# Kernel tuning notes

Measured on AMD Instinct MI355X. Metric: run time of the kernel, lower is better.

The kernel has to match this reference:

```python
import jax, jax.numpy as jnp
import numpy as np
import math

STRIDES = {"p3": 8, "p4": 16, "p5": 32}
STRIDE_SCALE = 4
ASPECT_RATIOS = (0.5, 1.0, 2.0)
SCALE_CLAMP = math.log(224.0 / 8.0)
IOU_LOW, IOU_HIGH = 0.3, 0.6
IMG = 784.0


def _make_locations(hw, stride):
    # centers of feature cells projected to image coords
    xs = (jnp.arange(hw, dtype=jnp.float32) + 0.5) * stride
    gy, gx = jnp.meshgrid(xs, xs, indexing="ij")
    return jnp.stack([gx.ravel(), gy.ravel()], axis=1)  # (H*W, 2)


def setup_inputs() -> dict:
    key = jax.random.key(0)
    k1, k2 = jax.random.split(key)
    locations_p3 = _make_locations(98, 8)
    locations_p4 = _make_locations(49, 16)
    locations_p5 = _make_locations(25, 32)
    n_anchors = (9604 + 2401 + 625) * 3  # 37890
    deltas = jax.random.normal(k1, (n_anchors, 4), dtype=jnp.float32) * 0.2
    # GT boxes (M,5): x1,y1,x2,y2,class ; make valid boxes
    km1, km2, km3 = jax.random.split(k2, 3)
    xy1 = jax.random.uniform(km1, (64, 2), minval=0.0, maxval=IMG * 0.7)
    wh = jax.random.uniform(km2, (64, 2), minval=16.0, maxval=IMG * 0.3)
    cls = jax.random.randint(km3, (64, 1), 0, 20).astype(jnp.float32)
    gt_boxes = jnp.concatenate([xy1, xy1 + wh, cls], axis=1)
    return {
        "locations_p3": locations_p3,
        "locations_p4": locations_p4,
        "locations_p5": locations_p5,
        "deltas": deltas,
        "gt_boxes": gt_boxes,
    }


def _anchors_for_level(locations, stride):
    # locations: (L, 2)
    area = (STRIDE_SCALE * stride) ** 2
    boxes = []
    for ar in ASPECT_RATIOS:
        w = math.sqrt(area / ar)
        h = area / w
        xc, yc = locations[:, 0], locations[:, 1]
        boxes.append(jnp.stack([xc - w / 2.0, yc - h / 2.0,
                                xc + w / 2.0, yc + h / 2.0], axis=1))
    # (A, L, 4) -> (L, A, 4) -> (L*A, 4)
    return jnp.stack(boxes).transpose(1, 0, 2).reshape(-1, 4)


def _apply_deltas(deltas, anchors):
    dx, dy = deltas[:, 0], deltas[:, 1]
    dw = jnp.minimum(deltas[:, 2], SCALE_CLAMP)
    dh = jnp.minimum(deltas[:, 3], SCALE_CLAMP)
    wa = anchors[:, 2] - anchors[:, 0]
    ha = anchors[:, 3] - anchors[:, 1]
    xa = anchors[:, 0] + wa / 2.0
    ya = anchors[:, 1] + ha / 2.0
    xp = dx * wa + xa
    yp = dy * ha + ya
    wp = jnp.exp(dw) * wa
    hp = jnp.exp(dh) * ha
    return jnp.stack([xp - wp / 2.0, yp - hp / 2.0,
                      xp + wp / 2.0, yp + hp / 2.0], axis=1)


def _iou(b1, b2):
    a1 = (b1[:, 2] - b1[:, 0]) * (b1[:, 3] - b1[:, 1])
    a2 = (b2[:, 2] - b2[:, 0]) * (b2[:, 3] - b2[:, 1])
    lt = jnp.maximum(b1[:, None, :2], b2[None, :, :2])
    rb = jnp.minimum(b1[:, None, 2:], b2[None, :, 2:])
    wh = jnp.clip(rb - lt, 0.0)
    inter = wh[:, :, 0] * wh[:, :, 1]
    union = a1[:, None] + a2[None, :] - inter
    return inter / union


def _get_deltas(anchors, gt_boxes4):
    invalid = gt_boxes4[:, 0] < 0
    wa = anchors[:, 2] - anchors[:, 0]
    ha = anchors[:, 3] - anchors[:, 1]
    xa = anchors[:, 0] + wa / 2.0
    ya = anchors[:, 1] + ha / 2.0
    wg = jnp.clip(gt_boxes4[:, 2] - gt_boxes4[:, 0], 1.0)
    hg = jnp.clip(gt_boxes4[:, 3] - gt_boxes4[:, 1], 1.0)
    xg = gt_boxes4[:, 0] + wg / 2.0
    yg = gt_boxes4[:, 1] + hg / 2.0
    d = jnp.stack([(xg - xa) / wa, (yg - ya) / ha,
                   jnp.log(wg / wa), jnp.log(hg / ha)], axis=1)
    return jnp.where(invalid[:, None], -1e8, d)


def _match(anchors, gt_boxes):
    # gt_boxes: (M,5). Assume all valid (class != -1) per setup.
    m = _iou(anchors, gt_boxes[:, :4])  # (N, M)
    idx = jnp.argmax(m, axis=1)
    quality = jnp.max(m, axis=1)
    matched = gt_boxes[idx]  # (N, 5)
    matched = jnp.where((quality <= IOU_LOW)[:, None], -1.0, matched)
    neutral = (quality > IOU_LOW) & (quality < IOU_HIGH)
    matched = jnp.where(neutral[:, None], -1e8, matched)
    return matched


def reference(locations_p3, locations_p4, locations_p5, deltas, gt_boxes):
    a3 = _anchors_for_level(locations_p3, STRIDES["p3"])
    a4 = _anchors_for_level(locations_p4, STRIDES["p4"])
    a5 = _anchors_for_level(locations_p5, STRIDES["p5"])
    anchors = jnp.concatenate([a3, a4, a5], axis=0)  # (N, 4)
    proposals = _apply_deltas(deltas, anchors)       # (N, 4)
    matched_gt = _match(anchors, gt_boxes)           # (N, 5)
    gt_deltas = _get_deltas(anchors, matched_gt[:, :4])  # (N, 4)
    return proposals, matched_gt, gt_deltas
```

## Files before the change

kernel.cpp:

```cpp
#include <hip/hip_runtime.h>
#include <math.h>

#define N_LOC3 9604
#define N_LOC4 2401
#define N_LOC5 625
#define N_A3   28812
#define N_A4   36015
#define N_TOTAL 37890
#define N_GT   64

#define SCALE_CLAMP_F 3.3322045101752038f
#define SENTINEL (-100000000.0f)

__global__ __launch_bounds__(256) void rpn_fused_kernel(
    const float* __restrict__ loc3,
    const float* __restrict__ loc4,
    const float* __restrict__ loc5,
    const float* __restrict__ deltas,
    const float* __restrict__ gt,
    float* __restrict__ out)
{
    __shared__ float sgt[N_GT * 5];
    __shared__ float sarea[N_GT];

    const int tid = threadIdx.x;
    for (int i = tid; i < N_GT * 5; i += blockDim.x) sgt[i] = gt[i];
    __syncthreads();
    if (tid < N_GT) {
        sarea[tid] = (sgt[tid*5 + 2] - sgt[tid*5 + 0]) * (sgt[tid*5 + 3] - sgt[tid*5 + 1]);
    }
    __syncthreads();

    const int a = blockIdx.x * blockDim.x + tid;
    if (a >= N_TOTAL) return;

    int stride_i, rel;
    const float* loc;
    if (a < N_A3)      { stride_i = 8;  loc = loc3; rel = a; }
    else if (a < N_A4) { stride_i = 16; loc = loc4; rel = a - N_A3; }
    else               { stride_i = 32; loc = loc5; rel = a - N_A4; }
    const int li = rel / 3;
    const int ar = rel - li * 3;

    const float2 xy = ((const float2*)loc)[li];
    const float xc = xy.x, yc = xy.y;

    const double s4   = 4.0 * (double)stride_i;
    const double area = s4 * s4;
    const double ard  = (ar == 0) ? 0.5 : (ar == 1 ? 1.0 : 2.0);
    const double wd   = sqrt(area / ard);
    const double hd   = area / wd;
    const float hw = (float)(wd * 0.5);
    const float hh = (float)(hd * 0.5);

    const float x1 = xc - hw, y1 = yc - hh;
    const float x2 = xc + hw, y2 = yc + hh;

    const float wa = x2 - x1;
    const float ha = y2 - y1;
    const float xa = x1 + wa * 0.5f;
    const float ya = y1 + ha * 0.5f;

    const float4 d = ((const float4*)deltas)[a];
    const float dw = fminf(d.z, SCALE_CLAMP_F);
    const float dh = fminf(d.w, SCALE_CLAMP_F);
    const float xp = d.x * wa + xa;
    const float yp = d.y * ha + ya;
    const float wp = expf(dw) * wa;
    const float hp = expf(dh) * ha;
    float4 prop;
    prop.x = xp - wp * 0.5f;
    prop.y = yp - hp * 0.5f;
    prop.z = xp + wp * 0.5f;
    prop.w = yp + hp * 0.5f;
    ((float4*)out)[a] = prop;

    const float a1 = wa * ha;
    float best = -1.0f;
    int bidx = 0;
    #pragma unroll 8
    for (int j = 0; j < N_GT; ++j) {
        const float gx1 = sgt[j*5 + 0];
        const float gy1 = sgt[j*5 + 1];
        const float gx2 = sgt[j*5 + 2];
        const float gy2 = sgt[j*5 + 3];
        const float ltx = fmaxf(x1, gx1);
        const float lty = fmaxf(y1, gy1);
        const float rbx = fminf(x2, gx2);
        const float rby = fminf(y2, gy2);
        const float iw = fmaxf(rbx - ltx, 0.0f);
        const float ih = fmaxf(rby - lty, 0.0f);
        const float inter = iw * ih;
        const float uni = a1 + sarea[j] - inter;
        const float iou = inter / uni;
        if (iou > best) { best = iou; bidx = j; }
    }

    float m0, m1, m2, m3, m4;
    if (best <= 0.3f) {
        m0 = m1 = m2 = m3 = m4 = -1.0f;
    } else if (best < 0.6f) {
        m0 = m1 = m2 = m3 = m4 = SENTINEL;
    } else {
        m0 = sgt[bidx*5 + 0];
        m1 = sgt[bidx*5 + 1];
        m2 = sgt[bidx*5 + 2];
        m3 = sgt[bidx*5 + 3];
        m4 = sgt[bidx*5 + 4];
    }
    float* mout = out + N_TOTAL * 4 + a * 5;
    mout[0] = m0; mout[1] = m1; mout[2] = m2; mout[3] = m3; mout[4] = m4;

    float o0, o1, o2, o3;
    if (m0 < 0.0f) {
        o0 = o1 = o2 = o3 = SENTINEL;
    } else {
        const float wg = fmaxf(m2 - m0, 1.0f);
        const float hg = fmaxf(m3 - m1, 1.0f);
        const float xg = m0 + wg * 0.5f;
        const float yg = m1 + hg * 0.5f;
        o0 = (xg - xa) / wa;
        o1 = (yg - ya) / ha;
        o2 = logf(wg / wa);
        o3 = logf(hg / ha);
    }
    float* gout = out + N_TOTAL * 9 + a * 4;
    gout[0] = o0; gout[1] = o1; gout[2] = o2; gout[3] = o3;
}

extern "C" void kernel_launch(void* const* d_in, const int* in_sizes, int n_in,
                              void* d_out, int out_size, void* d_ws, size_t ws_size,
                              hipStream_t stream) {
    const float* loc3   = (const float*)d_in[0];
    const float* loc4   = (const float*)d_in[1];
    const float* loc5   = (const float*)d_in[2];
    const float* deltas = (const float*)d_in[3];
    const float* gt     = (const float*)d_in[4];
    float* out = (float*)d_out;

    const int block = 256;
    const int grid = (N_TOTAL + block - 1) / block;
    rpn_fused_kernel<<<grid, block, 0, stream>>>(loc3, loc4, loc5, deltas, gt, out);
}
```

Baseline: 72.70 us.

## Split GT matching across four lanes per anchor with shuffle reduction

Each anchor is now handled by four threads. Each thread scans 16 of the 64 GT boxes, and the four partial results are combined with xor shuffles. The IoU comparison uses cross-multiplication in place of a division per box, and anchor half-sizes are computed on the host instead of with per-thread double-precision sqrt. Output writes are split across the sub-lanes, which quadruples the thread count and makes the proposal and delta math redundant across the four lanes. The cross-multiplied comparison may break ties differently from the per-box division.

New measurement: 68.08 us. -6.4%, faster.

```diff
diff --git a/kernel.cpp b/kernel.cpp
--- a/kernel.cpp
+++ b/kernel.cpp
@@ -1,65 +1,114 @@
 #include <hip/hip_runtime.h>
 #include <math.h>
 
-#define N_LOC3 9604
-#define N_LOC4 2401
-#define N_LOC5 625
-#define N_A3   28812
-#define N_A4   36015
+#define N_A3    28812
+#define N_A4    36015
 #define N_TOTAL 37890
-#define N_GT   64
+#define N_GT    64
 
 #define SCALE_CLAMP_F 3.3322045101752038f
 #define SENTINEL (-100000000.0f)
 
-__global__ __launch_bounds__(256) void rpn_fused_kernel(
+__global__ __launch_bounds__(256) void rpn_fused_v2(
     const float* __restrict__ loc3,
     const float* __restrict__ loc4,
     const float* __restrict__ loc5,
     const float* __restrict__ deltas,
     const float* __restrict__ gt,
-    float* __restrict__ out)
+    float* __restrict__ out,
+    float hw_a, float hh_a,
+    float hw_c, float hh_c)
 {
     __shared__ float sgt[N_GT * 5];
     __shared__ float sarea[N_GT];
 
     const int tid = threadIdx.x;
-    for (int i = tid; i < N_GT * 5; i += blockDim.x) sgt[i] = gt[i];
-    __syncthreads();
     if (tid < N_GT) {
-        sarea[tid] = (sgt[tid*5 + 2] - sgt[tid*5 + 0]) * (sgt[tid*5 + 3] - sgt[tid*5 + 1]);
+        const float g0 = gt[tid * 5 + 0];
+        const float g1 = gt[tid * 5 + 1];
+        const float g2 = gt[tid * 5 + 2];
+        const float g3 = gt[tid * 5 + 3];
+        const float g4 = gt[tid * 5 + 4];
+        sgt[tid * 5 + 0] = g0; sgt[tid * 5 + 1] = g1; sgt[tid * 5 + 2] = g2;
+        sgt[tid * 5 + 3] = g3; sgt[tid * 5 + 4] = g4;
+        sarea[tid] = (g2 - g0) * (g3 - g1);
     }
     __syncthreads();
 
-    const int a = blockIdx.x * blockDim.x + tid;
+    const int gidx = blockIdx.x * 256 + tid;
+    const int a    = gidx >> 2;
+    const int sub  = tid & 3;
     if (a >= N_TOTAL) return;
 
-    int stride_i, rel;
+    int rel, lvl;
     const float* loc;
-    if (a < N_A3)      { stride_i = 8;  loc = loc3; rel = a; }
-    else if (a < N_A4) { stride_i = 16; loc = loc4; rel = a - N_A3; }
-    else               { stride_i = 32; loc = loc5; rel = a - N_A4; }
+    if (a < N_A3)      { lvl = 0; loc = loc3; rel = a; }
+    else if (a < N_A4) { lvl = 1; loc = loc4; rel = a - N_A3; }
+    else               { lvl = 2; loc = loc5; rel = a - N_A4; }
     const int li = rel / 3;
     const int ar = rel - li * 3;
 
     const float2 xy = ((const float2*)loc)[li];
-    const float xc = xy.x, yc = xy.y;
+    const float scale = (float)(1 << lvl);
+    const float hw = (ar == 0 ? hw_a : (ar == 1 ? 16.0f : hw_c)) * scale;
+    const float hh = (ar == 0 ? hh_a : (ar == 1 ? 16.0f : hh_c)) * scale;
 
-    const double s4   = 4.0 * (double)stride_i;
-    const double area = s4 * s4;
-    const double ard  = (ar == 0) ? 0.5 : (ar == 1 ? 1.0 : 2.0);
-    const double wd   = sqrt(area / ard);
-    const double hd   = area / wd;
-    const float hw = (float)(wd * 0.5);
-    const float hh = (float)(hd * 0.5);
+    const float x1 = xy.x - hw, y1 = xy.y - hh;
+    const float x2 = xy.x + hw, y2 = xy.y + hh;
+    const float wa = x2 - x1, ha = y2 - y1;
+    const float xa = x1 + wa * 0.5f, ya = y1 + ha * 0.5f;
+    const float a1 = wa * ha;
 
-    const float x1 = xc - hw, y1 = yc - hh;
-    const float x2 = xc + hw, y2 = yc + hh;
+    int   bj;
+    float bi, bu;
+    {
+        const int j0 = sub * 16;
+        {
+            const float ltx = fmaxf(x1, sgt[j0 * 5 + 0]);
+            const float lty = fmaxf(y1, sgt[j0 * 5 + 1]);
+            const float rbx = fminf(x2, sgt[j0 * 5 + 2]);
+            const float rby = fminf(y2, sgt[j0 * 5 + 3]);
+            const float iw = fmaxf(rbx - ltx, 0.0f);
+            const float ih = fmaxf(rby - lty, 0.0f);
+            bi = iw * ih;
+            bu = a1 + sarea[j0] - bi;
+            bj = j0;
+        }
+        #pragma unroll
+        for (int k = 1; k < 16; ++k) {
+            const int j = j0 + k;
+            const float ltx = fmaxf(x1, sgt[j * 5 + 0]);
+            const float lty = fmaxf(y1, sgt[j * 5 + 1]);
+            const float rbx = fminf(x2, sgt[j * 5 + 2]);
+            const float rby = fminf(y2, sgt[j * 5 + 3]);
+            const float iw = fmaxf(rbx - ltx, 0.0f);
+            const float ih = fmaxf(rby - lty, 0.0f);
+            const float inter = iw * ih;
+            const float uni = a1 + sarea[j] - inter;
+            if (inter * bu > bi * uni) { bi = inter; bu = uni; bj = j; }
+        }
+    }
+    #pragma unroll
+    for (int s = 1; s < 4; s <<= 1) {
+        const float oi = __shfl_xor(bi, s, 64);
+        const float ou = __shfl_xor(bu, s, 64);
+        const int   oj = __shfl_xor(bj, s, 64);
+        const float p_o = oi * bu, p_b = bi * ou;
+        if (p_o > p_b || (p_o == p_b && oj < bj)) { bi = oi; bu = ou; bj = oj; }
+    }
 
-    const float wa = x2 - x1;
-    const float ha = y2 - y1;
-    const float xa = x1 + wa * 0.5f;
-    const float ya = y1 + ha * 0.5f;
+    const float q = bi / bu;
+
+    float m0, m1, m2, m3, m4;
+    if (q <= 0.3f) {
+        m0 = m1 = m2 = m3 = m4 = -1.0f;
+    } else if (q < 0.6f) {
+        m0 = m1 = m2 = m3 = m4 = SENTINEL;
+    } else {
+        const int off = bj * 5;
+        m0 = sgt[off + 0]; m1 = sgt[off + 1]; m2 = sgt[off + 2];
+        m3 = sgt[off + 3]; m4 = sgt[off + 4];
+    }
 
     const float4 d = ((const float4*)deltas)[a];
     const float dw = fminf(d.z, SCALE_CLAMP_F);
@@ -73,43 +122,6 @@
     prop.y = yp - hp * 0.5f;
     prop.z = xp + wp * 0.5f;
     prop.w = yp + hp * 0.5f;
-    ((float4*)out)[a] = prop;
-
-    const float a1 = wa * ha;
-    float best = -1.0f;
-    int bidx = 0;
-    #pragma unroll 8
-    for (int j = 0; j < N_GT; ++j) {
-        const float gx1 = sgt[j*5 + 0];
-        const float gy1 = sgt[j*5 + 1];
-        const float gx2 = sgt[j*5 + 2];
-        const float gy2 = sgt[j*5 + 3];
-        const float ltx = fmaxf(x1, gx1);
-        const float lty = fmaxf(y1, gy1);
-        const float rbx = fminf(x2, gx2);
-        const float rby = fminf(y2, gy2);
-        const float iw = fmaxf(rbx - ltx, 0.0f);
-        const float ih = fmaxf(rby - lty, 0.0f);
-        const float inter = iw * ih;
-        const float uni = a1 + sarea[j] - inter;
-        const float iou = inter / uni;
-        if (iou > best) { best = iou; bidx = j; }
-    }
-
-    float m0, m1, m2, m3, m4;
-    if (best <= 0.3f) {
-        m0 = m1 = m2 = m3 = m4 = -1.0f;
-    } else if (best < 0.6f) {
-        m0 = m1 = m2 = m3 = m4 = SENTINEL;
-    } else {
-        m0 = sgt[bidx*5 + 0];
-        m1 = sgt[bidx*5 + 1];
-        m2 = sgt[bidx*5 + 2];
-        m3 = sgt[bidx*5 + 3];
-        m4 = sgt[bidx*5 + 4];
-    }
-    float* mout = out + N_TOTAL * 4 + a * 5;
-    mout[0] = m0; mout[1] = m1; mout[2] = m2; mout[3] = m3; mout[4] = m4;
 
     float o0, o1, o2, o3;
     if (m0 < 0.0f) {
@@ -124,8 +136,17 @@
         o2 = logf(wg / wa);
         o3 = logf(hg / ha);
     }
-    float* gout = out + N_TOTAL * 9 + a * 4;
-    gout[0] = o0; gout[1] = o1; gout[2] = o2; gout[3] = o3;
+
+    if (sub == 0) {
+        ((float4*)out)[a] = prop;
+    } else if (sub == 1) {
+        float* mout = out + N_TOTAL * 4 + a * 5;
+        mout[0] = m0; mout[1] = m1; mout[2] = m2; mout[3] = m3; mout[4] = m4;
+    } else if (sub == 2) {
+        float* g = out + N_TOTAL * 9 + a * 4;
+        ((float2*)g)[0] = make_float2(o0, o1);
+        ((float2*)g)[1] = make_float2(o2, o3);
+    }
 }
 
 extern "C" void kernel_launch(void* const* d_in, const int* in_sizes, int n_in,
@@ -138,7 +159,13 @@
     const float* gt     = (const float*)d_in[4];
     float* out = (float*)d_out;
 
+    const double w05 = sqrt(1024.0 / 0.5), h05 = 1024.0 / w05;
+    const double w20 = sqrt(1024.0 / 2.0), h20 = 1024.0 / w20;
+    const float hw_a = (float)(w05 * 0.5), hh_a = (float)(h05 * 0.5);
+    const float hw_c = (float)(w20 * 0.5), hh_c = (float)(h20 * 0.5);
+
     const int block = 256;
-    const int grid = (N_TOTAL + block - 1) / block;
-    rpn_fused_kernel<<<grid, block, 0, stream>>>(loc3, loc4, loc5, deltas, gt, out);
+    const int grid = (N_TOTAL * 4 + block - 1) / block;
+    rpn_fused_v2<<<grid, block, 0, stream>>>(loc3, loc4, loc5, deltas, gt, out,
+                                             hw_a, hh_a, hw_c, hh_c);
 }
```
